# Performance work log

Measured on AMD Instinct MI355X. Metric: run time of the kernel, lower is better.

## Reference

```python
import jax, jax.numpy as jnp
import numpy as np


def _gcn_conv(x, src, dst, W, b, num_nodes, deg_inv_sqrt):
    # PyG GCNConv: h = x @ W, then normalized scatter-add over edges (incl. self loops), + bias
    h = x @ W  # [N, d_out]
    norm = deg_inv_sqrt[src] * deg_inv_sqrt[dst]  # [E']
    msg = h[src] * norm[:, None]  # gather + scale, [E', d_out]
    out = jax.ops.segment_sum(msg, dst, num_segments=num_nodes)  # scatter-add to targets
    return out + b


def reference(x, edge_index, W1, b1, W2, b2, num_nodes):
    src0, dst0 = edge_index[0], edge_index[1]
    loop = jnp.arange(num_nodes, dtype=edge_index.dtype)
    # add self loops (PyG default add_self_loops=True)
    src = jnp.concatenate([src0, loop])
    dst = jnp.concatenate([dst0, loop])
    # symmetric normalization D^{-1/2} (A+I) D^{-1/2}, degree from self-looped graph
    deg = jax.ops.segment_sum(jnp.ones_like(src, dtype=x.dtype), dst, num_segments=num_nodes)
    deg_inv_sqrt = jnp.where(deg > 0, jax.lax.rsqrt(jnp.maximum(deg, 1)), 0.0).astype(x.dtype)

    z = jax.nn.relu(_gcn_conv(x, src, dst, W1, b1, num_nodes, deg_inv_sqrt))
    z = jax.nn.relu(_gcn_conv(z, src, dst, W2, b2, num_nodes, deg_inv_sqrt))
    return z


def setup_inputs() -> dict:
    key = jax.random.key(0)
    k1, k2, k3, k4 = jax.random.split(key, 4)
    N, E, D, H = 50000, 1600000, 128, 128
    x = jax.random.normal(k1, (N, D), dtype=jnp.float32)
    edge_index = jax.random.randint(k2, (2, E), 0, N, dtype=jnp.int64)
    s = 1.0 / np.sqrt(D)
    W1 = jax.random.normal(k3, (D, H), dtype=jnp.float32) * s
    W2 = jax.random.normal(k4, (H, H), dtype=jnp.float32) * s
    return {
        "x": x,
        "edge_index": edge_index,
        "W1": W1,
        "b1": jnp.zeros((H,), jnp.float32),
        "W2": W2,
        "b2": jnp.zeros((H,), jnp.float32),
        "num_nodes": N,
    }
```

## Files before the change

### kernel.cpp

```cpp
#include <hip/hip_runtime.h>

#define FD 128
#define BSH 7
#define BPAD 16
#define CH 4096
#define CHT 16

typedef __attribute__((ext_vector_type(8))) short bf16x8;
typedef __attribute__((ext_vector_type(4))) float f32x4;

__device__ inline unsigned bfr(float f) {
    unsigned u = __float_as_uint(f);
    return (u + 0x7FFF + ((u >> 16) & 1)) >> 16;
}
__device__ inline float uplo(unsigned p) { return __uint_as_float(p << 16); }
__device__ inline float uphi(unsigned p) { return __uint_as_float(p & 0xFFFF0000u); }


__global__ __launch_bounds__(256) void hist_kernel(
        const int* __restrict__ dst, int* __restrict__ bhist, int E, int K) {
    __shared__ int lh[512];
    for (int i = threadIdx.x; i < K; i += 256) lh[i] = 0;
    __syncthreads();
    for (int e = blockIdx.x * 256 + threadIdx.x; e < E; e += gridDim.x * 256)
        atomicAdd(&lh[dst[e] >> BSH], 1);
    __syncthreads();
    for (int i = threadIdx.x; i < K; i += 256)
        if (lh[i]) atomicAdd(&bhist[i], lh[i]);
}

__global__ __launch_bounds__(512) void bscan_kernel(
        const int* __restrict__ bhist, int* __restrict__ bbase, int* __restrict__ bcur,
        int* __restrict__ rp, int K, int E, int N) {
    __shared__ int sm[512];
    int t = threadIdx.x;
    int v = (t < K) ? bhist[t] : 0;
    sm[t] = v;
    __syncthreads();
    for (int off = 1; off < 512; off <<= 1) {
        int add = (t >= off) ? sm[t - off] : 0;
        __syncthreads();
        sm[t] += add;
        __syncthreads();
    }
    if (t < K) { bbase[t] = sm[t] - v; bcur[t * BPAD] = sm[t] - v; }
    if (t == 0) { bbase[K] = E; rp[N] = E; }
}

__global__ __launch_bounds__(256) void partition_kernel(
        const int* __restrict__ src, const int* __restrict__ dst,
        int* __restrict__ bcur, int* __restrict__ pairs, int E) {
    __shared__ int   lcnt[512];
    __shared__ int   lstart[512];
    __shared__ int   ldelta[512];
    __shared__ int   sm[256];
    __shared__ int   staged[CH];
    __shared__ short binof[CH];
    int t = threadIdx.x;
    int base = blockIdx.x * CH;
    int n = min(CH, E - base);

    lcnt[t] = 0; lcnt[t + 256] = 0;
    __syncthreads();

    int pk[CHT]; int bn[CHT];
    #pragma unroll
    for (int j = 0; j < CHT; ++j) {
        int i = t + j * 256;
        bn[j] = -1;
        if (i < n) {
            int d = dst[base + i];
            int s = src[base + i];
            bn[j] = d >> BSH;
            pk[j] = ((d & ((1 << BSH) - 1)) << 17) | s;
            atomicAdd(&lcnt[bn[j]], 1);
        }
    }
    __syncthreads();

    int c0 = lcnt[2 * t], c1 = lcnt[2 * t + 1];
    int s2 = c0 + c1;
    sm[t] = s2;
    __syncthreads();
    for (int off = 1; off < 256; off <<= 1) {
        int add = (t >= off) ? sm[t - off] : 0;
        __syncthreads();
        sm[t] += add;
        __syncthreads();
    }
    int ex = sm[t] - s2;
    lstart[2 * t] = ex;     lstart[2 * t + 1] = ex + c0;
    lcnt[2 * t]   = ex;     lcnt[2 * t + 1]   = ex + c0;
    __syncthreads();

    #pragma unroll
    for (int j = 0; j < CHT; ++j) {
        if (bn[j] >= 0) {
            int pos = atomicAdd(&lcnt[bn[j]], 1);
            staged[pos] = pk[j];
            binof[pos] = (short)bn[j];
        }
    }
    __syncthreads();

    #pragma unroll
    for (int k = 0; k < 2; ++k) {
        int b = 2 * t + k;
        int cnt = lcnt[b] - lstart[b];
        if (cnt > 0) {
            int g = atomicAdd(&bcur[b * BPAD], cnt);
            ldelta[b] = g - lstart[b];
        }
    }
    __syncthreads();

    for (int i = t; i < n; i += 256)
        pairs[ldelta[binof[i]] + i] = staged[i];
}

__global__ __launch_bounds__(256) void build_kernel(
        const int* __restrict__ pairs, const int* __restrict__ bbase,
        int* __restrict__ rp, float* __restrict__ dis, int* __restrict__ col, int N) {
    __shared__ int lcnt[1 << BSH];
    __shared__ int lsum[1 << BSH];
    __shared__ int lbase[1 << BSH];
    int b = blockIdx.x;
    int t = threadIdx.x;
    int nbase = b << BSH;
    int nn = min(1 << BSH, N - nbase);
    int beg = bbase[b], end = bbase[b + 1];
    if (t < 128) lcnt[t] = 0;
    __syncthreads();
    for (int e = beg + t; e < end; e += 256)
        atomicAdd(&lcnt[pairs[e] >> 17], 1);
    __syncthreads();
    if (t < 128) lsum[t] = lcnt[t];
    __syncthreads();
    for (int off = 1; off < 128; off <<= 1) {
        int add = (t < 128 && t >= off) ? lsum[t - off] : 0;
        __syncthreads();
        if (t < 128) lsum[t] += add;
        __syncthreads();
    }
    if (t < 128) {
        int excl = beg + lsum[t] - lcnt[t];
        lbase[t] = excl;
        if (t < nn) {
            rp[nbase + t] = excl;
            dis[nbase + t] = rsqrtf((float)(lcnt[t] + 1));
        }
    }
    __syncthreads();
    if (t < 128) lcnt[t] = lbase[t];
    __syncthreads();
    for (int e = beg + t; e < end; e += 256) {
        int p = pairs[e];
        int pos = atomicAdd(&lcnt[p >> 17], 1);
        col[pos] = p & 0x1FFFF;
    }
}


__global__ void wt_kernel(const float* __restrict__ W1, unsigned short* __restrict__ W1T,
                          const float* __restrict__ W2, unsigned short* __restrict__ W2T) {
    int k = blockIdx.x & (FD - 1);
    int n = threadIdx.x;
    if (blockIdx.x < FD) W1T[n * FD + k] = (unsigned short)bfr(W1[k * FD + n]);
    else                 W2T[n * FD + k] = (unsigned short)bfr(W2[k * FD + n]);
}


#define APAD 8
#define ASTR (FD + APAD)

template <bool A32>
__device__ void gemm_body(const void* __restrict__ Ap,
                          const unsigned short* __restrict__ WT,
                          const float* __restrict__ dis,
                          unsigned short* __restrict__ C, int M) {
    __shared__ unsigned short As[128 * ASTR];
    __shared__ unsigned short Bs[128 * ASTR];
    int tid = threadIdx.x;
    int lane = tid & 63;
    int wave = tid >> 6;
    int quad = lane >> 4;
    int l16 = lane & 15;
    int rowBase = blockIdx.x * 128;

    #pragma unroll
    for (int p = 0; p < 8; ++p) {
        int r = p * 16 + (tid >> 4);
        int cq = (tid & 15) * 8;
        int gr = rowBase + r;
        uint4 v = make_uint4(0u, 0u, 0u, 0u);
        if (A32) {
            if (gr < M) {
                const float* a = (const float*)Ap + (size_t)gr * FD + cq;
                float4 f0 = *(const float4*)a;
                float4 f1 = *(const float4*)(a + 4);
                v.x = bfr(f0.x) | (bfr(f0.y) << 16);
                v.y = bfr(f0.z) | (bfr(f0.w) << 16);
                v.z = bfr(f1.x) | (bfr(f1.y) << 16);
                v.w = bfr(f1.z) | (bfr(f1.w) << 16);
            }
        } else {
            if (gr < M) v = *(const uint4*)((const unsigned short*)Ap + (size_t)gr * FD + cq);
        }
        *(uint4*)&As[r * ASTR + cq] = v;
        *(uint4*)&Bs[r * ASTR + cq] = *(const uint4*)&WT[(size_t)r * FD + cq];
    }
    __syncthreads();

    int m0 = wave * 32;
    f32x4 acc[2][8] = {};
    #pragma unroll
    for (int kt = 0; kt < 4; ++kt) {
        int ko = kt * 32 + quad * 8;
        bf16x8 a0 = *(bf16x8*)&As[(m0 + l16) * ASTR + ko];
        bf16x8 a1 = *(bf16x8*)&As[(m0 + 16 + l16) * ASTR + ko];
        #pragma unroll
        for (int n = 0; n < 8; ++n) {
            bf16x8 b = *(bf16x8*)&Bs[(n * 16 + l16) * ASTR + ko];
            acc[0][n] = __builtin_amdgcn_mfma_f32_16x16x32_bf16(a0, b, acc[0][n], 0, 0, 0);
            acc[1][n] = __builtin_amdgcn_mfma_f32_16x16x32_bf16(a1, b, acc[1][n], 0, 0, 0);
        }
    }

    #pragma unroll
    for (int ms = 0; ms < 2; ++ms) {
        #pragma unroll
        for (int r = 0; r < 4; ++r) {
            int grow = rowBase + m0 + ms * 16 + quad * 4 + r;
            if (grow < M) {
                float dv = dis[grow];
                #pragma unroll
                for (int n = 0; n < 8; ++n) {
                    C[(size_t)grow * FD + n * 16 + l16] =
                        (unsigned short)bfr(dv * acc[ms][n][r]);
                }
            }
        }
    }
}

__global__ __launch_bounds__(256) void gemm_mfma_f32(
        const float* __restrict__ A, const unsigned short* __restrict__ WT,
        const float* __restrict__ dis, unsigned short* __restrict__ C, int M) {
    gemm_body<true>(A, WT, dis, C, M);
}

__global__ __launch_bounds__(256) void gemm_mfma_bf16(
        const unsigned short* __restrict__ A, const unsigned short* __restrict__ WT,
        const float* __restrict__ dis, unsigned short* __restrict__ C, int M) {
    gemm_body<false>(A, WT, dis, C, M);
}


__global__ __launch_bounds__(256) void agg_kernel(
        const unsigned* __restrict__ h, const float* __restrict__ dis,
        const int* __restrict__ rp, const int* __restrict__ col,
        const float2* __restrict__ bias, void* __restrict__ out, int N, int obf) {
    int v = blockIdx.x * 4 + threadIdx.y;
    v = __builtin_amdgcn_readfirstlane(v);
    if (v >= N) return;
    int t = threadIdx.x;
    float dv = dis[v];
    size_t vb = (size_t)v * 64 + t;
    unsigned hp = h[vb];
    float2 acc;
    acc.x = uplo(hp); acc.y = uphi(hp);
    int e = rp[v];
    int end = rp[v + 1];

    for (; e + 16 <= end; e += 16) {
        int u[16];
        #pragma unroll
        for (int j = 0; j < 16; ++j) u[j] = col[e + j];
        unsigned p[16];
        #pragma unroll
        for (int j = 0; j < 16; ++j) p[j] = h[(size_t)u[j] * 64 + t];
        #pragma unroll
        for (int j = 0; j < 16; ++j) {
            acc.x += uplo(p[j]); acc.y += uphi(p[j]);
        }
    }
    for (; e + 4 <= end; e += 4) {
        int u0 = col[e], u1 = col[e + 1], u2 = col[e + 2], u3 = col[e + 3];
        unsigned p0 = h[(size_t)u0 * 64 + t];
        unsigned p1 = h[(size_t)u1 * 64 + t];
        unsigned p2 = h[(size_t)u2 * 64 + t];
        unsigned p3 = h[(size_t)u3 * 64 + t];
        acc.x += uplo(p0); acc.y += uphi(p0);
        acc.x += uplo(p1); acc.y += uphi(p1);
        acc.x += uplo(p2); acc.y += uphi(p2);
        acc.x += uplo(p3); acc.y += uphi(p3);
    }
    for (; e < end; ++e) {
        unsigned p = h[(size_t)col[e] * 64 + t];
        acc.x += uplo(p); acc.y += uphi(p);
    }

    float2 bb = bias[t];
    float2 r;
    r.x = fmaxf(fmaf(dv, acc.x, bb.x), 0.0f);
    r.y = fmaxf(fmaf(dv, acc.y, bb.y), 0.0f);
    if (obf) {
        ((unsigned*)out)[vb] = bfr(r.x) | (bfr(r.y) << 16);
    } else {
        ((float2*)out)[vb] = r;
    }
}


extern "C" void kernel_launch(void* const* d_in, const int* in_sizes, int n_in,
                              void* d_out, int out_size, void* d_ws, size_t ws_size,
                              hipStream_t stream) {
    const float* x  = (const float*)d_in[0];
    const int*   ei = (const int*)d_in[1];
    const float* W1 = (const float*)d_in[2];
    const float* b1 = (const float*)d_in[3];
    const float* W2 = (const float*)d_in[4];
    const float* b2 = (const float*)d_in[5];

    int N = in_sizes[0] / FD;
    int E = in_sizes[1] / 2;
    const int* src = ei;
    const int* dst = ei + E;
    int K = (N + (1 << BSH) - 1) >> BSH;

    char* base = (char*)d_ws;
    size_t off = 0;
    auto align256 = [](size_t v) { return (v + 255) & ~(size_t)255; };
    int*            rp    = (int*)(base + off);            off += align256((size_t)(N + 1) * 4);
    float*          dis   = (float*)(base + off);          off += align256((size_t)N * 4);
    int*            bhist = (int*)(base + off);            off += align256(512 * 4);
    int*            bbase = (int*)(base + off);            off += align256(513 * 4);
    int*            bcur  = (int*)(base + off);            off += align256((size_t)K * BPAD * 4);
    unsigned short* w1t   = (unsigned short*)(base + off); off += align256((size_t)FD * FD * 2);
    unsigned short* w2t   = (unsigned short*)(base + off); off += align256((size_t)FD * FD * 2);
    int*            col   = (int*)(base + off);            off += align256((size_t)E * 4);
    unsigned short* hbuf  = (unsigned short*)(base + off); off += align256((size_t)N * FD * 2);
    unsigned short* z1    = (unsigned short*)(base + off); off += align256((size_t)N * FD * 2);
    int*            pairs = (int*)(base + off);            off += align256((size_t)E * 4);
    (void)ws_size; (void)n_in; (void)out_size;

    int PB = (E + CH - 1) / CH;

    (void)hipMemsetAsync(bhist, 0, 512 * 4, stream);
    hist_kernel     <<<512, 256, 0, stream>>>(dst, bhist, E, K);
    bscan_kernel    <<<1, 512, 0, stream>>>(bhist, bbase, bcur, rp, K, E, N);
    partition_kernel<<<PB, 256, 0, stream>>>(src, dst, bcur, pairs, E);
    build_kernel    <<<K, 256, 0, stream>>>(pairs, bbase, rp, dis, col, N);

    wt_kernel<<<2 * FD, FD, 0, stream>>>(W1, w1t, W2, w2t);

    dim3 aggBlk(64, 4);
    int aggGrid = (N + 3) / 4;
    int gemmGrid = (N + 127) / 128;

    gemm_mfma_f32 <<<gemmGrid, 256, 0, stream>>>(x, w1t, dis, hbuf, N);
    agg_kernel<<<aggGrid, aggBlk, 0, stream>>>((const unsigned*)hbuf, dis, rp, col,
                                               (const float2*)b1, z1, N, 1);
    gemm_mfma_bf16<<<gemmGrid, 256, 0, stream>>>(z1, w2t, dis, hbuf, N);
    agg_kernel<<<aggGrid, aggBlk, 0, stream>>>((const unsigned*)hbuf, dis, rp, col,
                                               (const float2*)b2, d_out, N, 0);
}
```

Before: 259.8 us.

## Split feature matrix into two 64-column planes and stage build pairs in LDS

The GEMM now writes h in a planar layout of two 64-feature halves, each N x 64 bf16. The aggregation kernel runs a second grid dimension over these halves, and each wave handles two edges at once, with 32 lanes gathering 128-byte rows per edge. The partial sums are combined with a cross-half shuffle before the self-loop, bias and ReLU. The second GEMM reads this planar input. The build kernel caches each bucket's pairs in shared memory so pairs is not read twice from global memory. The planar split is meant to make each gathered row half as wide, improving cache locality for the random neighbour gathers, at the cost of reading col twice and launching twice as many aggregation blocks.

```diff
diff --git a/kernel.cpp b/kernel.cpp
--- a/kernel.cpp
+++ b/kernel.cpp
@@ -5,6 +5,7 @@
 #define BPAD 16
 #define CH 4096
 #define CHT 16
+#define SCAP 6144
 
 typedef __attribute__((ext_vector_type(8))) short bf16x8;
 typedef __attribute__((ext_vector_type(4))) float f32x4;
@@ -121,6 +122,7 @@
 __global__ __launch_bounds__(256) void build_kernel(
         const int* __restrict__ pairs, const int* __restrict__ bbase,
         int* __restrict__ rp, float* __restrict__ dis, int* __restrict__ col, int N) {
+    __shared__ int staged[SCAP];
     __shared__ int lcnt[1 << BSH];
     __shared__ int lsum[1 << BSH];
     __shared__ int lbase[1 << BSH];
@@ -129,10 +131,13 @@
     int nbase = b << BSH;
     int nn = min(1 << BSH, N - nbase);
     int beg = bbase[b], end = bbase[b + 1];
+    int cnt = end - beg;
+    int sc = min(cnt, SCAP);
+    for (int i = t; i < sc; i += 256) staged[i] = pairs[beg + i];
     if (t < 128) lcnt[t] = 0;
     __syncthreads();
-    for (int e = beg + t; e < end; e += 256)
-        atomicAdd(&lcnt[pairs[e] >> 17], 1);
+    for (int i = t; i < sc; i += 256) atomicAdd(&lcnt[staged[i] >> 17], 1);
+    for (int i = SCAP + t; i < cnt; i += 256) atomicAdd(&lcnt[pairs[beg + i] >> 17], 1);
     __syncthreads();
     if (t < 128) lsum[t] = lcnt[t];
     __syncthreads();
@@ -153,8 +158,13 @@
     __syncthreads();
     if (t < 128) lcnt[t] = lbase[t];
     __syncthreads();
-    for (int e = beg + t; e < end; e += 256) {
-        int p = pairs[e];
+    for (int i = t; i < sc; i += 256) {
+        int p = staged[i];
+        int pos = atomicAdd(&lcnt[p >> 17], 1);
+        col[pos] = p & 0x1FFFF;
+    }
+    for (int i = SCAP + t; i < cnt; i += 256) {
+        int p = pairs[beg + i];
         int pos = atomicAdd(&lcnt[p >> 17], 1);
         col[pos] = p & 0x1FFFF;
     }
@@ -173,7 +183,7 @@
 #define APAD 8
 #define ASTR (FD + APAD)
 
-template <bool A32>
+template <bool A32, bool PLANARA>
 __device__ void gemm_body(const void* __restrict__ Ap,
                           const unsigned short* __restrict__ WT,
                           const float* __restrict__ dis,
@@ -186,6 +196,7 @@
     int quad = lane >> 4;
     int l16 = lane & 15;
     int rowBase = blockIdx.x * 128;
+    size_t plane = (size_t)M * 64;
 
     #pragma unroll
     for (int p = 0; p < 8; ++p) {
@@ -203,6 +214,12 @@
                 v.z = bfr(f1.x) | (bfr(f1.y) << 16);
                 v.w = bfr(f1.z) | (bfr(f1.w) << 16);
             }
+        } else if (PLANARA) {
+            if (gr < M) {
+                const unsigned short* a = (const unsigned short*)Ap
+                    + (size_t)(cq >> 6) * plane + (size_t)gr * 64 + (cq & 63);
+                v = *(const uint4*)a;
+            }
         } else {
             if (gr < M) v = *(const uint4*)((const unsigned short*)Ap + (size_t)gr * FD + cq);
         }
@@ -235,7 +252,8 @@
                 float dv = dis[grow];
                 #pragma unroll
                 for (int n = 0; n < 8; ++n) {
-                    C[(size_t)grow * FD + n * 16 + l16] =
+                    int f = n * 16 + l16;
+                    C[(size_t)(f >> 6) * plane + (size_t)grow * 64 + (f & 63)] =
                         (unsigned short)bfr(dv * acc[ms][n][r]);
                 }
             }
@@ -246,13 +264,13 @@
 __global__ __launch_bounds__(256) void gemm_mfma_f32(
         const float* __restrict__ A, const unsigned short* __restrict__ WT,
         const float* __restrict__ dis, unsigned short* __restrict__ C, int M) {
-    gemm_body<true>(A, WT, dis, C, M);
-}
-
-__global__ __launch_bounds__(256) void gemm_mfma_bf16(
+    gemm_body<true, false>(A, WT, dis, C, M);
+}
+
+__global__ __launch_bounds__(256) void gemm_mfma_pl(
         const unsigned short* __restrict__ A, const unsigned short* __restrict__ WT,
         const float* __restrict__ dis, unsigned short* __restrict__ C, int M) {
-    gemm_body<false>(A, WT, dis, C, M);
+    gemm_body<false, true>(A, WT, dis, C, M);
 }
 
 
@@ -263,51 +281,57 @@
     int v = blockIdx.x * 4 + threadIdx.y;
     v = __builtin_amdgcn_readfirstlane(v);
     if (v >= N) return;
+    int ph = blockIdx.y;
+    const unsigned* hp = h + (size_t)ph * N * 32;
     int t = threadIdx.x;
-    float dv = dis[v];
-    size_t vb = (size_t)v * 64 + t;
-    unsigned hp = h[vb];
-    float2 acc;
-    acc.x = uplo(hp); acc.y = uphi(hp);
+    int fl = t & 31;
+    int eo = t >> 5;
+    float2 acc = make_float2(0.f, 0.f);
     int e = rp[v];
     int end = rp[v + 1];
 
     for (; e + 16 <= end; e += 16) {
-        int u[16];
-        #pragma unroll
-        for (int j = 0; j < 16; ++j) u[j] = col[e + j];
-        unsigned p[16];
-        #pragma unroll
-        for (int j = 0; j < 16; ++j) p[j] = h[(size_t)u[j] * 64 + t];
-        #pragma unroll
-        for (int j = 0; j < 16; ++j) {
-            acc.x += uplo(p[j]); acc.y += uphi(p[j]);
-        }
-    }
-    for (; e + 4 <= end; e += 4) {
-        int u0 = col[e], u1 = col[e + 1], u2 = col[e + 2], u3 = col[e + 3];
-        unsigned p0 = h[(size_t)u0 * 64 + t];
-        unsigned p1 = h[(size_t)u1 * 64 + t];
-        unsigned p2 = h[(size_t)u2 * 64 + t];
-        unsigned p3 = h[(size_t)u3 * 64 + t];
-        acc.x += uplo(p0); acc.y += uphi(p0);
-        acc.x += uplo(p1); acc.y += uphi(p1);
-        acc.x += uplo(p2); acc.y += uphi(p2);
-        acc.x += uplo(p3); acc.y += uphi(p3);
-    }
-    for (; e < end; ++e) {
-        unsigned p = h[(size_t)col[e] * 64 + t];
+        int u[8];
+        #pragma unroll
+        for (int j = 0; j < 8; ++j) {
+            int a = col[e + 2 * j];
+            int b = col[e + 2 * j + 1];
+            u[j] = eo ? b : a;
+        }
+        unsigned p[8];
+        #pragma unroll
+        for (int j = 0; j < 8; ++j) p[j] = hp[(size_t)u[j] * 32 + fl];
+        #pragma unroll
+        for (int j = 0; j < 8; ++j) { acc.x += uplo(p[j]); acc.y += uphi(p[j]); }
+    }
+    for (; e + 2 <= end; e += 2) {
+        int a = col[e], b = col[e + 1];
+        int uu = eo ? b : a;
+        unsigned p = hp[(size_t)uu * 32 + fl];
         acc.x += uplo(p); acc.y += uphi(p);
     }
-
-    float2 bb = bias[t];
-    float2 r;
-    r.x = fmaxf(fmaf(dv, acc.x, bb.x), 0.0f);
-    r.y = fmaxf(fmaf(dv, acc.y, bb.y), 0.0f);
-    if (obf) {
-        ((unsigned*)out)[vb] = bfr(r.x) | (bfr(r.y) << 16);
-    } else {
-        ((float2*)out)[vb] = r;
+    if (e < end && eo == 0) {
+        unsigned p = hp[(size_t)col[e] * 32 + fl];
+        acc.x += uplo(p); acc.y += uphi(p);
+    }
+
+    acc.x += __shfl_xor(acc.x, 32);
+    acc.y += __shfl_xor(acc.y, 32);
+
+    if (eo == 0) {
+        unsigned sp = hp[(size_t)v * 32 + fl];
+        acc.x += uplo(sp); acc.y += uphi(sp);
+        float dv = dis[v];
+        float2 bb = bias[32 * ph + fl];
+        float2 r;
+        r.x = fmaxf(fmaf(dv, acc.x, bb.x), 0.0f);
+        r.y = fmaxf(fmaf(dv, acc.y, bb.y), 0.0f);
+        if (obf) {
+            ((unsigned*)out)[(size_t)ph * N * 32 + (size_t)v * 32 + fl] =
+                bfr(r.x) | (bfr(r.y) << 16);
+        } else {
+            ((float2*)out)[(size_t)v * 64 + 32 * ph + fl] = r;
+        }
     }
 }
 
@@ -355,13 +379,13 @@
     wt_kernel<<<2 * FD, FD, 0, stream>>>(W1, w1t, W2, w2t);
 
     dim3 aggBlk(64, 4);
-    int aggGrid = (N + 3) / 4;
+    dim3 aggGrid((N + 3) / 4, 2);
     int gemmGrid = (N + 127) / 128;
 
-    gemm_mfma_f32 <<<gemmGrid, 256, 0, stream>>>(x, w1t, dis, hbuf, N);
+    gemm_mfma_f32<<<gemmGrid, 256, 0, stream>>>(x, w1t, dis, hbuf, N);
     agg_kernel<<<aggGrid, aggBlk, 0, stream>>>((const unsigned*)hbuf, dis, rp, col,
                                                (const float2*)b1, z1, N, 1);
-    gemm_mfma_bf16<<<gemmGrid, 256, 0, stream>>>(z1, w2t, dis, hbuf, N);
+    gemm_mfma_pl <<<gemmGrid, 256, 0, stream>>>(z1, w2t, dis, hbuf, N);
     agg_kernel<<<aggGrid, aggBlk, 0, stream>>>((const unsigned*)hbuf, dis, rp, col,
                                                (const float2*)b2, d_out, N, 0);
 }
```

Result: slower. 280.0 us (+7.8%).

## Replace global-histogram binning with per-block local sort and gather-based CSR build

Applied to the files above, without the earlier changes.

Drops the separate histogram pass and the global atomic bucket cursor. Each partition block now sorts its chunk locally in place and records its per-bucket offsets in a table. The build kernel then gathers each bucket's segments from every partition block, staging them in LDS when they fit, before building the CSR. This removes one full pass over dst and the contended global atomics, at the cost of many small, poorly coalesced serial segment reads per thread in the build kernel. The offset table reuses the hbuf workspace.

```diff
diff --git a/kernel.cpp b/kernel.cpp
--- a/kernel.cpp
+++ b/kernel.cpp
@@ -2,9 +2,10 @@
 
 #define FD 128
 #define BSH 7
-#define BPAD 16
-#define CH 4096
-#define CHT 16
+#define CH 2048
+#define CHT 8
+#define KMAX 512
+#define SCAP 8192
 
 typedef __attribute__((ext_vector_type(8))) short bf16x8;
 typedef __attribute__((ext_vector_type(4))) float f32x4;
@@ -17,45 +18,14 @@
 __device__ inline float uphi(unsigned p) { return __uint_as_float(p & 0xFFFF0000u); }
 
 
-__global__ __launch_bounds__(256) void hist_kernel(
-        const int* __restrict__ dst, int* __restrict__ bhist, int E, int K) {
-    __shared__ int lh[512];
-    for (int i = threadIdx.x; i < K; i += 256) lh[i] = 0;
-    __syncthreads();
-    for (int e = blockIdx.x * 256 + threadIdx.x; e < E; e += gridDim.x * 256)
-        atomicAdd(&lh[dst[e] >> BSH], 1);
-    __syncthreads();
-    for (int i = threadIdx.x; i < K; i += 256)
-        if (lh[i]) atomicAdd(&bhist[i], lh[i]);
-}
-
-__global__ __launch_bounds__(512) void bscan_kernel(
-        const int* __restrict__ bhist, int* __restrict__ bbase, int* __restrict__ bcur,
-        int* __restrict__ rp, int K, int E, int N) {
-    __shared__ int sm[512];
-    int t = threadIdx.x;
-    int v = (t < K) ? bhist[t] : 0;
-    sm[t] = v;
-    __syncthreads();
-    for (int off = 1; off < 512; off <<= 1) {
-        int add = (t >= off) ? sm[t - off] : 0;
-        __syncthreads();
-        sm[t] += add;
-        __syncthreads();
-    }
-    if (t < K) { bbase[t] = sm[t] - v; bcur[t * BPAD] = sm[t] - v; }
-    if (t == 0) { bbase[K] = E; rp[N] = E; }
-}
-
 __global__ __launch_bounds__(256) void partition_kernel(
         const int* __restrict__ src, const int* __restrict__ dst,
-        int* __restrict__ bcur, int* __restrict__ pairs, int E) {
-    __shared__ int   lcnt[512];
-    __shared__ int   lstart[512];
-    __shared__ int   ldelta[512];
-    __shared__ int   sm[256];
-    __shared__ int   staged[CH];
-    __shared__ short binof[CH];
+        int* __restrict__ lstartG, int* __restrict__ total,
+        int* __restrict__ pairs, int E, int K) {
+    __shared__ int lcnt[KMAX];
+    __shared__ int lstart[KMAX];
+    __shared__ int sm[256];
+    __shared__ int staged[CH];
     int t = threadIdx.x;
     int base = blockIdx.x * CH;
     int n = min(CH, E - base);
@@ -98,42 +68,96 @@
         if (bn[j] >= 0) {
             int pos = atomicAdd(&lcnt[bn[j]], 1);
             staged[pos] = pk[j];
-            binof[pos] = (short)bn[j];
-        }
-    }
-    __syncthreads();
-
-    #pragma unroll
-    for (int k = 0; k < 2; ++k) {
-        int b = 2 * t + k;
-        int cnt = lcnt[b] - lstart[b];
-        if (cnt > 0) {
-            int g = atomicAdd(&bcur[b * BPAD], cnt);
-            ldelta[b] = g - lstart[b];
         }
     }
     __syncthreads();
 
     for (int i = t; i < n; i += 256)
-        pairs[ldelta[binof[i]] + i] = staged[i];
+        pairs[base + i] = staged[i];
+
+    size_t lrow = (size_t)blockIdx.x * (K + 1);
+    for (int b = t; b < K; b += 256) {
+        lstartG[lrow + b] = lstart[b];
+        int c = lcnt[b] - lstart[b];
+        if (c) atomicAdd(&total[b], c);
+    }
+    if (t == 0) lstartG[lrow + K] = n;
+}
+
+__global__ __launch_bounds__(512) void totscan_kernel(
+        const int* __restrict__ total, int* __restrict__ bbase,
+        int* __restrict__ rp, int K, int E, int N) {
+    __shared__ int sm[512];
+    int t = threadIdx.x;
+    int v = (t < K) ? total[t] : 0;
+    sm[t] = v;
+    __syncthreads();
+    for (int off = 1; off < 512; off <<= 1) {
+        int add = (t >= off) ? sm[t - off] : 0;
+        __syncthreads();
+        sm[t] += add;
+        __syncthreads();
+    }
+    if (t < K) bbase[t] = sm[t] - v;
+    if (t == 0) { bbase[K] = E; rp[N] = E; }
 }
 
 __global__ __launch_bounds__(256) void build_kernel(
-        const int* __restrict__ pairs, const int* __restrict__ bbase,
-        int* __restrict__ rp, float* __restrict__ dis, int* __restrict__ col, int N) {
+        const int* __restrict__ pairs, const int* __restrict__ lstartG,
+        const int* __restrict__ bbase, int* __restrict__ rp,
+        float* __restrict__ dis, int* __restrict__ col, int N, int PB, int K) {
+    __shared__ int staged[SCAP];
     __shared__ int lcnt[1 << BSH];
     __shared__ int lsum[1 << BSH];
     __shared__ int lbase[1 << BSH];
+    __shared__ int sm[256];
     int b = blockIdx.x;
     int t = threadIdx.x;
     int nbase = b << BSH;
     int nn = min(1 << BSH, N - nbase);
-    int beg = bbase[b], end = bbase[b + 1];
+    int beg = bbase[b];
+    int cnt = bbase[b + 1] - beg;
+
+    int fp[4], fl0[4], flen[4];
+    int nf = 0, mysum = 0;
+    for (int p = t; p < PB; p += 256) {
+        size_t lrow = (size_t)p * (K + 1);
+        int l0 = lstartG[lrow + b];
+        int l1 = lstartG[lrow + b + 1];
+        fp[nf] = p; fl0[nf] = l0; flen[nf] = l1 - l0;
+        mysum += l1 - l0;
+        ++nf;
+    }
+    sm[t] = mysum;
+    __syncthreads();
+    for (int off = 1; off < 256; off <<= 1) {
+        int add = (t >= off) ? sm[t - off] : 0;
+        __syncthreads();
+        sm[t] += add;
+        __syncthreads();
+    }
+    int o = sm[t] - mysum;
+
     if (t < 128) lcnt[t] = 0;
-    __syncthreads();
-    for (int e = beg + t; e < end; e += 256)
-        atomicAdd(&lcnt[pairs[e] >> 17], 1);
-    __syncthreads();
+
+    if (cnt <= SCAP) {
+        for (int f = 0; f < nf; ++f) {
+            int gbase = fp[f] * CH + fl0[f];
+            for (int i = 0; i < flen[f]; ++i) staged[o + i] = pairs[gbase + i];
+            o += flen[f];
+        }
+        __syncthreads();
+        for (int i = t; i < cnt; i += 256) atomicAdd(&lcnt[staged[i] >> 17], 1);
+    } else {
+        __syncthreads();
+        for (int f = 0; f < nf; ++f) {
+            int gbase = fp[f] * CH + fl0[f];
+            for (int i = 0; i < flen[f]; ++i)
+                atomicAdd(&lcnt[pairs[gbase + i] >> 17], 1);
+        }
+    }
+    __syncthreads();
+
     if (t < 128) lsum[t] = lcnt[t];
     __syncthreads();
     for (int off = 1; off < 128; off <<= 1) {
@@ -153,10 +177,22 @@
     __syncthreads();
     if (t < 128) lcnt[t] = lbase[t];
     __syncthreads();
-    for (int e = beg + t; e < end; e += 256) {
-        int p = pairs[e];
-        int pos = atomicAdd(&lcnt[p >> 17], 1);
-        col[pos] = p & 0x1FFFF;
+
+    if (cnt <= SCAP) {
+        for (int i = t; i < cnt; i += 256) {
+            int p = staged[i];
+            int pos = atomicAdd(&lcnt[p >> 17], 1);
+            col[pos] = p & 0x1FFFF;
+        }
+    } else {
+        for (int f = 0; f < nf; ++f) {
+            int gbase = fp[f] * CH + fl0[f];
+            for (int i = 0; i < flen[f]; ++i) {
+                int p = pairs[gbase + i];
+                int pos = atomicAdd(&lcnt[p >> 17], 1);
+                col[pos] = p & 0x1FFFF;
+            }
+        }
     }
 }
 
@@ -327,30 +363,28 @@
     const int* src = ei;
     const int* dst = ei + E;
     int K = (N + (1 << BSH) - 1) >> BSH;
+    int PB = (E + CH - 1) / CH;
 
     char* base = (char*)d_ws;
     size_t off = 0;
     auto align256 = [](size_t v) { return (v + 255) & ~(size_t)255; };
     int*            rp    = (int*)(base + off);            off += align256((size_t)(N + 1) * 4);
     float*          dis   = (float*)(base + off);          off += align256((size_t)N * 4);
-    int*            bhist = (int*)(base + off);            off += align256(512 * 4);
+    int*            total = (int*)(base + off);            off += align256(512 * 4);
     int*            bbase = (int*)(base + off);            off += align256(513 * 4);
-    int*            bcur  = (int*)(base + off);            off += align256((size_t)K * BPAD * 4);
     unsigned short* w1t   = (unsigned short*)(base + off); off += align256((size_t)FD * FD * 2);
     unsigned short* w2t   = (unsigned short*)(base + off); off += align256((size_t)FD * FD * 2);
     int*            col   = (int*)(base + off);            off += align256((size_t)E * 4);
     unsigned short* hbuf  = (unsigned short*)(base + off); off += align256((size_t)N * FD * 2);
     unsigned short* z1    = (unsigned short*)(base + off); off += align256((size_t)N * FD * 2);
     int*            pairs = (int*)(base + off);            off += align256((size_t)E * 4);
+    int*            lstartG = (int*)hbuf;
     (void)ws_size; (void)n_in; (void)out_size;
 
-    int PB = (E + CH - 1) / CH;
-
-    (void)hipMemsetAsync(bhist, 0, 512 * 4, stream);
-    hist_kernel     <<<512, 256, 0, stream>>>(dst, bhist, E, K);
-    bscan_kernel    <<<1, 512, 0, stream>>>(bhist, bbase, bcur, rp, K, E, N);
-    partition_kernel<<<PB, 256, 0, stream>>>(src, dst, bcur, pairs, E);
-    build_kernel    <<<K, 256, 0, stream>>>(pairs, bbase, rp, dis, col, N);
+    (void)hipMemsetAsync(total, 0, 512 * 4, stream);
+    partition_kernel<<<PB, 256, 0, stream>>>(src, dst, lstartG, total, pairs, E, K);
+    totscan_kernel  <<<1, 512, 0, stream>>>(total, bbase, rp, K, E, N);
+    build_kernel    <<<K, 256, 0, stream>>>(pairs, lstartG, bbase, rp, dis, col, N, PB, K);
 
     wt_kernel<<<2 * FD, FD, 0, stream>>>(W1, w1t, W2, w2t);
 
```

Result: no change. 258.2 us (-0.6%).
